# Kernel tuning notes

Hardware: AMD Instinct MI355X
Metric: run time of the kernel (lower is better)

Reference implementation:

```python
import jax, jax.numpy as jnp
import numpy as np

LN_EPS = 1e-5


def conv2d(x, w, b, stride, pad):
    # x: NCHW, w: OIHW
    y = jax.lax.conv_general_dilated(
        x, w, (stride, stride), [(pad, pad), (pad, pad)],
        dimension_numbers=("NCHW", "OIHW", "NCHW"))
    return y + b[None, :, None, None]


def gdn(x, gamma, beta):
    # y_c = x_c / sqrt(beta_c + sum_j gamma_cj * x_j^2)  (1x1 conv on x^2)
    norm = jnp.einsum("bchw,dc->bdhw", x * x, gamma) + beta[None, :, None, None]
    return x / jnp.sqrt(norm)


def layernorm(x, w, b):
    mu = jnp.mean(x, axis=-1, keepdims=True)
    var = jnp.var(x, axis=-1, keepdims=True)
    return (x - mu) / jnp.sqrt(var + LN_EPS) * w + b


def setup_inputs() -> dict:
    key = jax.random.key(0)
    ks = jax.random.split(key, 16)
    r = lambda i, shape: (jax.random.normal(ks[i], shape) * 0.02).astype(jnp.float32)
    N, M, K, D = 128, 192, 192, 128
    return {
        "x_p": jax.random.normal(ks[0], (4, 16, 3, 64, 64), jnp.float32),
        "y_g": jax.random.normal(ks[1], (64, K, 32), jnp.float32),
        "conv1_w": r(2, (N, 3, 5, 5)), "conv1_b": jnp.zeros((N,), jnp.float32),
        "gamma1": (0.1 * jnp.eye(N) + 1e-3).astype(jnp.float32), "beta1": jnp.ones((N,), jnp.float32),
        "conv2_w": r(3, (N, N, 5, 5)), "conv2_b": jnp.zeros((N,), jnp.float32),
        "gamma2": (0.1 * jnp.eye(N) + 1e-3).astype(jnp.float32), "beta2": jnp.ones((N,), jnp.float32),
        "conv3_w": r(4, (M, N, 3, 3)), "conv3_b": jnp.zeros((M,), jnp.float32),
        "ln_q_w": jnp.ones((M,), jnp.float32), "ln_q_b": jnp.zeros((M,), jnp.float32),
        "ln_kv_w": jnp.ones((K,), jnp.float32), "ln_kv_b": jnp.zeros((K,), jnp.float32),
        "ln_out_w": jnp.ones((M,), jnp.float32), "ln_out_b": jnp.zeros((M,), jnp.float32),
        "Wq": r(5, (D, M)), "Wk": r(6, (D, K)), "v_w": r(7, (1, D)),
        "Wv": r(8, (M, K)), "out_w": r(9, (M, M)), "out_b": jnp.zeros((M,), jnp.float32),
    }


def reference(x_p, y_g, conv1_w, conv1_b, gamma1, beta1, conv2_w, conv2_b,
              gamma2, beta2, conv3_w, conv3_b, ln_q_w, ln_q_b, ln_kv_w, ln_kv_b,
              ln_out_w, ln_out_b, Wq, Wk, v_w, Wv, out_w, out_b):
    B, P, C, Hp, Wp = x_p.shape
    x = x_p.reshape(B * P, C, Hp, Wp)
    # local encoder: conv s2 -> GDN -> conv s2 -> GDN -> conv s1 k3
    x = gdn(conv2d(x, conv1_w, conv1_b, 2, 2), gamma1, beta1)
    x = gdn(conv2d(x, conv2_w, conv2_b, 2, 2), gamma2, beta2)
    y_local = conv2d(x, conv3_w, conv3_b, 1, 1)          # (BP, M, h, w)
    BP, M, h, w = y_local.shape
    q = y_local.reshape(BP, M, h * w).transpose(0, 2, 1)  # (BP, Tq, M)
    kv = y_g.reshape(BP, y_g.shape[1], -1).transpose(0, 2, 1)  # (BP, Tk, K)
    q = layernorm(q, ln_q_w, ln_q_b)
    kv = layernorm(kv, ln_kv_w, ln_kv_b)
    # Bahdanau additive attention
    q_proj = jnp.einsum("bqm,dm->bqd", q, Wq)            # (BP, Tq, D)
    k_proj = jnp.einsum("bkc,dc->bkd", kv, Wk)           # (BP, Tk, D)
    energy = jnp.einsum("bqkd,d->bqk",
                        jnp.tanh(q_proj[:, :, None, :] + k_proj[:, None, :, :]),
                        v_w[0])                           # (BP, Tq, Tk)
    alpha = jax.nn.softmax(energy, axis=-1)
    v_proj = jnp.einsum("bkc,mc->bkm", kv, Wv)           # (BP, Tk, M)
    context = jnp.einsum("bqk,bkm->bqm", alpha, v_proj)
    context = jnp.einsum("bqm,nm->bqn", context, out_w) + out_b
    fused = layernorm(q + context, ln_out_w, ln_out_b)
    return fused.transpose(0, 2, 1).reshape(BP, M, h, w)
```

## Files before the change

kernel.cpp:

```cpp
#include <hip/hip_runtime.h>
#include <cstddef>
#include <cstdint>


typedef __bf16 bf16x8 __attribute__((ext_vector_type(8)));
typedef float floatx4 __attribute__((ext_vector_type(4)));
typedef unsigned short ushortT;
typedef unsigned short ushort8v __attribute__((ext_vector_type(8)));

#if __has_builtin(__builtin_amdgcn_exp2f)
#define EXP2F(x) __builtin_amdgcn_exp2f(x)
#else
#define EXP2F(x) exp2f(x)
#endif
#if __has_builtin(__builtin_amdgcn_rcpf)
#define RCPF(x) __builtin_amdgcn_rcpf(x)
#else
#define RCPF(x) (1.f / (x))
#endif

__device__ __forceinline__ ushortT f2bf(float f) {
  unsigned u = __builtin_bit_cast(unsigned, f);
  unsigned r = (u + 0x7FFFu + ((u >> 16) & 1u)) >> 16;
  return (ushortT)r;
}
__device__ __forceinline__ float bf2f(ushortT u) {
  return __builtin_bit_cast(float, ((unsigned)u) << 16);
}

static constexpr size_t OFF_T1BF = 0;
static constexpr size_t OFF_X2BF = 4194304;
static constexpr size_t OFF_T2BF = 8388608;
static constexpr size_t OFF_X3BF = 9437184;
static constexpr size_t OFF_QRAW = 10485760;
static constexpr size_t OFF_WBQ  = 21299200;
static constexpr size_t OFF_WBK  = 21311488;
static constexpr size_t OFF_WBV  = 21323776;
static constexpr size_t OFF_WBO  = 21342208;
static constexpr size_t OFF_WT2  = 26079232;
static constexpr size_t OFF_WT3  = 26284032;
static constexpr size_t OFF_WC1  = 26394624;
static constexpr size_t OFF_GB1  = 26406912;
static constexpr size_t OFF_GB2  = 26415104;
static constexpr size_t OFF_KP   = OFF_T1BF;
static constexpr size_t OFF_VT   = OFF_T1BF + 262144;

__device__ __constant__ int d_TWI2[4][9] = {{ 0, 2, 4,10,12,14,20,22,24},
                                            { 1, 3,11,13,21,23, 0, 0, 0},
                                            { 5, 7, 9,15,17,19, 0, 0, 0},
                                            { 6, 8,16,18, 0, 0, 0, 0, 0}};
__device__ __constant__ int d_NT2[4] = {9, 6, 6, 4};

__device__ void dev_convw3(const float* w, ushortT* wt, int mode, int total,
                           int idx) {
  if (idx >= total) return;
  int j    = idx & 7;
  int om   = (idx >> 3) & 63;
  int kg   = (idx >> 9) & 3;
  int slab = idx >> 11;
  int mt, s, tap, T;
  if (mode == 0) {
    int ph;
    if (slab < 72) ph = 0; else if (slab < 120) ph = 1;
    else if (slab < 168) ph = 2; else ph = 3;
    const int st[4] = {0, 72, 120, 168};
    const int ns[4] = {36, 24, 24, 16};
    int rel = slab - st[ph];
    mt = rel / ns[ph]; s = rel % ns[ph];
    tap = d_TWI2[ph][s >> 2]; T = 25;
  } else {
    mt = slab / 36; s = slab % 36; tap = s >> 2; T = 9;
  }
  int cc = s & 3;
  int c  = cc * 32 + kg * 8 + j;
  int oc = mt * 64 + om;
  wt[idx] = f2bf(w[(size_t)(oc * 128 + c) * T + tap]);
}

__device__ void dev_convw1(const float* w, ushortT* wt, int idx) {
  if (idx >= 20480) return;
  int k    = idx & 31;
  int oc   = (idx >> 5) & 127;
  int slab = idx >> 12;
  int ph, i;
  if (slab < 2) { ph = 0; i = slab; } else { ph = slab - 1; i = 0; }
  int kg = k >> 3, jj = k & 7;
  int tidx = i * 8 + jj;
  float val = 0.f;
  if (kg < 3 && tidx < d_NT2[ph]) {
    int tap = d_TWI2[ph][tidx];
    val = w[(size_t)(oc * 3 + kg) * 25 + tap];
  }
  wt[idx] = f2bf(val);
}

__device__ void dev_wcast(const float* w, ushortT* wb, int total, float scale,
                          int idx) {
  if (idx < total) wb[idx] = f2bf(w[idx] * scale);
}

__global__ __launch_bounds__(256) void prep_kernel(
    const float* __restrict__ conv2_w, ushortT* __restrict__ wt2,
    const float* __restrict__ conv3_w, ushortT* __restrict__ wt3,
    const float* __restrict__ conv1_w, ushortT* __restrict__ wc1,
    const float* __restrict__ Wq, ushortT* __restrict__ wbq,
    const float* __restrict__ Wk, ushortT* __restrict__ wbk,
    const float* __restrict__ Wv, ushortT* __restrict__ wbv,
    const float* __restrict__ out_w, ushortT* __restrict__ wbo,
    const float* __restrict__ gamma1, ushortT* __restrict__ gb1,
    const float* __restrict__ gamma2, ushortT* __restrict__ gb2) {
  constexpr float C2LE = 2.88539008177792681f;
  int blk = blockIdx.x, tid = threadIdx.x;
  if (blk < 1600)      dev_convw3(conv2_w, wt2, 0, 409600, blk * 256 + tid);
  else if (blk < 2464) dev_convw3(conv3_w, wt3, 1, 221184, (blk - 1600) * 256 + tid);
  else if (blk < 2544) dev_convw1(conv1_w, wc1, (blk - 2464) * 256 + tid);
  else if (blk < 2640) dev_wcast(Wq, wbq, 24576, C2LE, (blk - 2544) * 256 + tid);
  else if (blk < 2736) dev_wcast(Wk, wbk, 24576, C2LE, (blk - 2640) * 256 + tid);
  else if (blk < 2880) dev_wcast(Wv, wbv, 36864, 1.f, (blk - 2736) * 256 + tid);
  else if (blk < 3024) dev_wcast(out_w, wbo, 36864, 1.f, (blk - 2880) * 256 + tid);
  else if (blk < 3088) dev_wcast(gamma1, gb1, 16384, 1.f, (blk - 3024) * 256 + tid);
  else                 dev_wcast(gamma2, gb2, 16384, 1.f, (blk - 3088) * 256 + tid);
}

__global__ __launch_bounds__(256, 1) void conv1_mfma_kernel(
    const float* __restrict__ x, const ushortT* __restrict__ wc1,
    const float* __restrict__ bias, ushortT* __restrict__ outb) {
  int b  = blockIdx.x >> 2;
  int yg = blockIdx.x & 3;
  int y0 = yg * 8;

  int wave = threadIdx.x >> 6;
  int lane = threadIdx.x & 63;
  int ln15 = lane & 15;
  int kg   = lane >> 4;
  int tid  = threadIdx.x;

  __shared__ ushortT simg[4680];
  __shared__ ushortT sA[5 * 128 * 40];

  for (int j = tid; j < 2340; j += 256) ((unsigned*)simg)[j] = 0u;
  __syncthreads();

  int ihBase = 2 * y0 - 2;
  const float* xb = x + (size_t)b * 3 * 4096;
  for (int j = tid; j < 960; j += 256) {
    int q = j & 15;
    int rr = j >> 4;
    int c = rr / 20, ihl = rr % 20;
    int ih = ihBase + ihl;
    if (ih >= 0 && ih < 64) {
      float4 v = *(const float4*)&xb[c * 4096 + ih * 64 + q * 4];
      int pr = ih & 1, u = ih >> 1;
      int lr = u - y0 + 1;
      int base0 = ((pr * 2 + 0) * 3 + c) * 360 + lr * 36;
      int base1 = ((pr * 2 + 1) * 3 + c) * 360 + lr * 36;
      simg[base0 + 2 * q + 1] = f2bf(v.x);
      simg[base1 + 2 * q + 1] = f2bf(v.y);
      simg[base0 + 2 * q + 2] = f2bf(v.z);
      simg[base1 + 2 * q + 2] = f2bf(v.w);
    }
  }
  for (int j = tid; j < 2560; j += 256) {
    int chunk = j & 3, row = j >> 2;
    uint4 v = *(const uint4*)&wc1[row * 32 + chunk * 8];
    *(uint4*)&sA[row * 40 + chunk * 8] = v;
  }
  __syncthreads();

  constexpr int TDR[4][9] = {{-1,-1,-1, 0, 0, 0, 1, 1, 1},
                             {-1,-1, 0, 0, 1, 1, 0, 0, 0},
                             {-1,-1,-1, 0, 0, 0, 0, 0, 0},
                             {-1,-1, 0, 0, 0, 0, 0, 0, 0}};
  constexpr int TDC[4][9] = {{-1, 0, 1,-1, 0, 1,-1, 0, 1},
                             {-1, 0,-1, 0,-1, 0, 0, 0, 0},
                             {-1, 0, 1,-1, 0, 1, 0, 0, 0},
                             {-1, 0,-1, 0, 0, 0, 0, 0, 0}};
  constexpr int NT[4]  = {9, 6, 6, 4};
  constexpr int NM[4]  = {2, 1, 1, 1};
  constexpr int SB[4]  = {0, 2, 3, 4};

  ushort8v Bf[4][5];
  #pragma unroll
  for (int ntl = 0; ntl < 4; ++ntl) {
    int ntg = wave * 4 + ntl;
    int yloc = ntg >> 1;
    int xx = (ntg & 1) * 16 + ln15;
    int lbase = (yloc + 1) * 36 + xx + 1 + kg * 360;
    #pragma unroll
    for (int ph = 0; ph < 4; ++ph) {
      int pbase = ph * 1080 + lbase;
      #pragma unroll
      for (int i = 0; i < 2; ++i) {
        if (i < NM[ph]) {
          ushort8v bv;
          #pragma unroll
          for (int j = 0; j < 8; ++j) {
            int tidx = i * 8 + j;
            if (tidx >= NT[ph]) tidx = 0;
            int off = TDR[ph][tidx] * 36 + TDC[ph][tidx];
            bv[j] = simg[pbase + off];
          }
          Bf[ntl][SB[ph] + i] = bv;
        }
      }
    }
  }

  #pragma unroll
  for (int m = 0; m < 8; ++m) {
    bf16x8 Af[5];
    #pragma unroll
    for (int s = 0; s < 5; ++s)
      Af[s] = *(const bf16x8*)&sA[(s * 128 + m * 16 + ln15) * 40 + kg * 8];
    int oc0 = m * 16 + kg * 4;
    float4 bv = *(const float4*)&bias[oc0];
    #pragma unroll
    for (int ntl = 0; ntl < 4; ++ntl) {
      floatx4 acc = (floatx4)0.f;
      #pragma unroll
      for (int s = 0; s < 5; ++s)
        acc = __builtin_amdgcn_mfma_f32_16x16x32_bf16(
            Af[s], __builtin_bit_cast(bf16x8, Bf[ntl][s]), acc, 0, 0, 0);
      int ntg = wave * 4 + ntl;
      int y = y0 + (ntg >> 1);
      int xx = (ntg & 1) * 16 + ln15;
      int p = y * 32 + xx;
      ushort4 o4 = {f2bf(acc[0] + bv.x), f2bf(acc[1] + bv.y),
                    f2bf(acc[2] + bv.z), f2bf(acc[3] + bv.w)};
      *(ushort4*)&outb[((size_t)b * 1024 + p) * 128 + oc0] = o4;
    }
  }
}

__global__ __launch_bounds__(256) void gdn_mfma_kernel(
    const ushortT* __restrict__ xbf, const ushortT* __restrict__ gb,
    const float* __restrict__ beta, ushortT* __restrict__ ybf,
    int HW, int nPixTiles, int isSplit) {
  int pt = blockIdx.x % nPixTiles;
  int b  = blockIdx.x / nPixTiles;
  int px0 = pt * 64;
  int tid = threadIdx.x;
  int wave = tid >> 6, lane = tid & 63, ln15 = lane & 15, kg = lane >> 4;

  __shared__ ushortT sG[128 * 136];
  __shared__ ushortT sX[64 * 136];

  for (int j = tid; j < 2048; j += 256) {
    int row = j >> 4, ch = j & 15;
    *(uint4*)&sG[row * 136 + ch * 8] = *(const uint4*)&gb[row * 128 + ch * 8];
  }
  for (int j = tid; j < 1024; j += 256) {
    int row = j >> 4, ch = j & 15;
    ushort8v xv = *(const ushort8v*)&xbf[((size_t)(b * HW + px0 + row)) * 128 + ch * 8];
    ushort8v sq;
    #pragma unroll
    for (int r = 0; r < 8; ++r) {
      float f = bf2f(xv[r]);
      sq[r] = f2bf(f * f);
    }
    *(ushort8v*)&sX[row * 136 + ch * 8] = sq;
  }
  __syncthreads();

  floatx4 acc[2][4];
  #pragma unroll
  for (int mi = 0; mi < 2; ++mi)
    #pragma unroll
    for (int nt = 0; nt < 4; ++nt) acc[mi][nt] = (floatx4)0.f;

  #pragma unroll
  for (int k0 = 0; k0 < 128; k0 += 32) {
    bf16x8 a0 = *(const bf16x8*)&sG[(wave * 32 + ln15) * 136 + k0 + kg * 8];
    bf16x8 a1 = *(const bf16x8*)&sG[(wave * 32 + 16 + ln15) * 136 + k0 + kg * 8];
    #pragma unroll
    for (int nt = 0; nt < 4; ++nt) {
      bf16x8 bb = *(const bf16x8*)&sX[(nt * 16 + ln15) * 136 + k0 + kg * 8];
      acc[0][nt] = __builtin_amdgcn_mfma_f32_16x16x32_bf16(a0, bb, acc[0][nt], 0, 0, 0);
      acc[1][nt] = __builtin_amdgcn_mfma_f32_16x16x32_bf16(a1, bb, acc[1][nt], 0, 0, 0);
    }
  }

  #pragma unroll
  for (int mi = 0; mi < 2; ++mi) {
    int d0 = wave * 32 + mi * 16 + kg * 4;
    float4 bt = *(const float4*)&beta[d0];
    #pragma unroll
    for (int nt = 0; nt < 4; ++nt) {
      int p = px0 + nt * 16 + ln15;
      ushort4 x4 = *(const ushort4*)&xbf[((size_t)(b * HW + p)) * 128 + d0];
      ushort4 o4;
      o4.x = f2bf(bf2f(x4.x) * rsqrtf(acc[mi][nt][0] + bt.x));
      o4.y = f2bf(bf2f(x4.y) * rsqrtf(acc[mi][nt][1] + bt.y));
      o4.z = f2bf(bf2f(x4.z) * rsqrtf(acc[mi][nt][2] + bt.z));
      o4.w = f2bf(bf2f(x4.w) * rsqrtf(acc[mi][nt][3] + bt.w));
      size_t dst;
      if (isSplit) {
        int h = p >> 5, w5 = p & 31;
        int ph = ((h & 1) << 1) | (w5 & 1);
        dst = (((size_t)b * 4 + ph) * 256 + (h >> 1) * 16 + (w5 >> 1)) * 128 + d0;
      } else {
        dst = ((size_t)b * 256 + p) * 128 + d0;
      }
      *(ushort4*)&ybf[dst] = o4;
    }
  }
}

template<int MODE>
__global__ __launch_bounds__(256, 2) void conv_mfma_kernel(
    const ushortT* __restrict__ X,
    const ushortT* __restrict__ Wt,
    const float* __restrict__ bias,
    ushortT* __restrict__ outb) {
  constexpr int OC  = (MODE == 0) ? 128 : 192;
  constexpr int NMT = OC / 64;
  constexpr int NPH = (MODE == 0) ? 4 : 1;

  int b   = blockIdx.x / (NMT * 4);
  int rem = blockIdx.x % (NMT * 4);
  int mt  = rem >> 2;
  int rs  = rem & 3;
  int r0  = rs * 4;

  int wave = threadIdx.x >> 6;
  int lane = threadIdx.x & 63;
  int ln15 = lane & 15;
  int kg   = lane >> 4;

  __shared__ ushortT simg[6 * 18 * 136];

  floatx4 acc[4];
  #pragma unroll
  for (int m = 0; m < 4; ++m) acc[m] = (floatx4)0.f;

  constexpr int NS2[4]      = {36, 24, 24, 16};
  constexpr int PHSTART2[4] = {0, 72, 120, 168};
  constexpr int TDR_2[4][9] = {{-1,-1,-1, 0, 0, 0, 1, 1, 1},
                               {-1,-1, 0, 0, 1, 1, 0, 0, 0},
                               {-1,-1,-1, 0, 0, 0, 0, 0, 0},
                               {-1,-1, 0, 0, 0, 0, 0, 0, 0}};
  constexpr int TDC_2[4][9] = {{-1, 0, 1,-1, 0, 1,-1, 0, 1},
                               {-1, 0,-1, 0,-1, 0, 0, 0, 0},
                               {-1, 0, 1,-1, 0, 1, 0, 0, 0},
                               {-1, 0,-1, 0, 0, 0, 0, 0, 0}};
  constexpr int TDR_3[9] = {-1,-1,-1, 0, 0, 0, 1, 1, 1};
  constexpr int TDC_3[9] = {-1, 0, 1,-1, 0, 1,-1, 0, 1};

  const int aoff = kg * 512 + ln15 * 8;
  uint4 apf[8][4];

  #pragma unroll
  for (int ph = 0; ph < NPH; ++ph) {
    const int NS = (MODE == 0) ? NS2[ph] : 36;
    const int slabBase = (MODE == 0) ? (PHSTART2[ph] + mt * NS2[ph]) : (mt * 36);
    const ushortT* wp0 = Wt + (size_t)slabBase * 2048 + aoff;

    __syncthreads();
    const ushortT* Xb = X + (((size_t)b * NPH + ph) * 256) * 128;
    for (int idx = threadIdx.x; idx < 1728; idx += 256) {
      int chunk = idx & 15;
      int pix = idx >> 4;
      int row = pix / 18, colm = pix - row * 18;
      int i = r0 - 1 + row, j = colm - 1;
      uint4 v = {0u, 0u, 0u, 0u};
      if (i >= 0 && i < 16 && j >= 0 && j < 16)
        v = *(const uint4*)(Xb + ((size_t)(i * 16 + j)) * 128 + chunk * 8);
      *(uint4*)&simg[(row * 18 + colm) * 136 + chunk * 8] = v;
    }
    #pragma unroll
    for (int jj = 0; jj < 8; ++jj)
      if (jj < NS) {
        #pragma unroll
        for (int m = 0; m < 4; ++m)
          apf[jj][m] = *(const uint4*)(wp0 + (size_t)jj * 2048 + m * 128);
      }
    __syncthreads();

    #pragma unroll
    for (int s0 = 0; s0 < NS; s0 += 8) {
      #pragma unroll
      for (int jj = 0; jj < 8; ++jj) {
        int s = s0 + jj;
        if (s < NS) {
          bf16x8 acur[4];
          #pragma unroll
          for (int m = 0; m < 4; ++m) acur[m] = __builtin_bit_cast(bf16x8, apf[jj][m]);
          int sp = s + 8;
          if (sp < NS) {
            #pragma unroll
            for (int m = 0; m < 4; ++m)
              apf[jj][m] = *(const uint4*)(wp0 + (size_t)sp * 2048 + m * 128);
          }
          int t  = s >> 2;
          int c0 = (s & 3) * 32;
          int dr = (MODE == 0) ? TDR_2[ph][t] : TDR_3[t];
          int dc = (MODE == 0) ? TDC_2[ph][t] : TDC_3[t];
          int lrow = wave + dr + 1;
          int lcol = ln15 + dc + 1;
          bf16x8 bfr = *(const bf16x8*)&simg[(lrow * 18 + lcol) * 136 + c0 + kg * 8];
          #pragma unroll
          for (int m = 0; m < 4; ++m)
            acc[m] = __builtin_amdgcn_mfma_f32_16x16x32_bf16(acur[m], bfr, acc[m], 0, 0, 0);
        }
      }
    }
  }

  #pragma unroll
  for (int m = 0; m < 4; ++m) {
    int mg = mt * 64 + m * 16 + kg * 4;
    float4 bv = *(const float4*)&bias[mg];
    int r = r0 + wave;
    int p = r * 16 + ln15;
    ushort4 o4 = {f2bf(acc[m][0] + bv.x), f2bf(acc[m][1] + bv.y),
                  f2bf(acc[m][2] + bv.z), f2bf(acc[m][3] + bv.w)};
    *(ushort4*)&outb[((size_t)b * 256 + p) * OC + mg] = o4;
  }
}

__global__ __launch_bounds__(256) void kv_prep_kernel(
    const float* __restrict__ yg, const float* __restrict__ ln_kv_w,
    const float* __restrict__ ln_kv_b, const ushortT* __restrict__ wbk,
    const ushortT* __restrict__ wbv, float* __restrict__ kp,
    ushortT* __restrict__ vT) {
  __shared__ float skvRaw[32 * 194];
  __shared__ ushortT skv[32 * 200];
  int b = blockIdx.x;
  int tid = threadIdx.x;
  int wave = tid >> 6, lane = tid & 63, ln15 = lane & 15, kg = lane >> 4;

  const float4* yg4 = (const float4*)(yg + (size_t)b * 6144);
  for (int j = tid; j < 1536; j += 256) {
    float4 v = yg4[j];
    int c = j >> 3;
    int t4 = (j & 7) * 4;
    skvRaw[(t4 + 0) * 194 + c] = v.x;
    skvRaw[(t4 + 1) * 194 + c] = v.y;
    skvRaw[(t4 + 2) * 194 + c] = v.z;
    skvRaw[(t4 + 3) * 194 + c] = v.w;
  }
  __syncthreads();
  for (int r = wave; r < 32; r += 4) {
    const float* src = skvRaw + r * 194;
    float v0 = src[lane], v1 = src[lane + 64], v2 = src[lane + 128];
    float s = v0 + v1 + v2;
    float s2 = v0 * v0 + v1 * v1 + v2 * v2;
    #pragma unroll
    for (int off = 32; off; off >>= 1) { s += __shfl_xor(s, off); s2 += __shfl_xor(s2, off); }
    float mean = s * (1.f / 192.f);
    float var = s2 * (1.f / 192.f) - mean * mean;
    float inv = rsqrtf(var + 1e-5f);
    skv[r * 200 + lane]       = f2bf((v0 - mean) * inv * ln_kv_w[lane]       + ln_kv_b[lane]);
    skv[r * 200 + lane + 64]  = f2bf((v1 - mean) * inv * ln_kv_w[lane + 64]  + ln_kv_b[lane + 64]);
    skv[r * 200 + lane + 128] = f2bf((v2 - mean) * inv * ln_kv_w[lane + 128] + ln_kv_b[lane + 128]);
  }
  __syncthreads();
  for (int ti = wave; ti < 40; ti += 4) {
    floatx4 acc = (floatx4)0.f;
    if (ti < 16) {
      int rt = ti >> 3, ct = ti & 7;
      #pragma unroll
      for (int k0 = 0; k0 < 192; k0 += 32) {
        bf16x8 afr = *(const bf16x8*)&skv[(rt * 16 + ln15) * 200 + k0 + kg * 8];
        bf16x8 bfr = *(const bf16x8*)&wbk[((size_t)(ct * 16 + ln15)) * 192 + k0 + kg * 8];
        acc = __builtin_amdgcn_mfma_f32_16x16x32_bf16(afr, bfr, acc, 0, 0, 0);
      }
      #pragma unroll
      for (int r = 0; r < 4; ++r)
        kp[((size_t)b * 32 + rt * 16 + kg * 4 + r) * 128 + ct * 16 + ln15] = acc[r];
    } else {
      int t2 = ti - 16;
      int rt = t2 / 12, ct = t2 % 12;
      #pragma unroll
      for (int k0 = 0; k0 < 192; k0 += 32) {
        bf16x8 afr = *(const bf16x8*)&skv[(rt * 16 + ln15) * 200 + k0 + kg * 8];
        bf16x8 bfr = *(const bf16x8*)&wbv[((size_t)(ct * 16 + ln15)) * 192 + k0 + kg * 8];
        acc = __builtin_amdgcn_mfma_f32_16x16x32_bf16(afr, bfr, acc, 0, 0, 0);
      }
      #pragma unroll
      for (int r = 0; r < 4; ++r)
        vT[((size_t)b * 192 + ct * 16 + ln15) * 32 + rt * 16 + kg * 4 + r] = f2bf(acc[r]);
    }
  }
}

__global__ __launch_bounds__(256) void attn_kernel(
    const ushortT* __restrict__ qrawb, const float* __restrict__ ln_q_w,
    const float* __restrict__ ln_q_b, const float* __restrict__ kp,
    const ushortT* __restrict__ vT, const ushortT* __restrict__ wbq,
    const ushortT* __restrict__ wbo, const float* __restrict__ vw,
    const float* __restrict__ out_b, const float* __restrict__ ln_out_w,
    const float* __restrict__ ln_out_b, float* __restrict__ out) {
  __shared__ ushortT smem[17284];
  ushortT* sqln = smem;
  float*   skp  = (float*)(smem + 3200);
  float*   sqpF = (float*)(smem + 11648);
  float*   se   = (float*)(smem + 15872);
  float*   swm  = (float*)(smem + 17024);
  float*   sS0  = (float*)(smem + 17280);
  ushortT* sctx = smem;
  float*   sf   = (float*)(smem + 3200);

  int b  = blockIdx.x >> 4;
  int t0 = (blockIdx.x & 15) * 16;
  int tid  = threadIdx.x;
  int wave = tid >> 6;
  int lane = tid & 63;
  int ln15 = lane & 15;
  int kg   = lane >> 4;

  {
    const float4* kp4 = (const float4*)(kp + (size_t)b * 4096);
    for (int j = tid; j < 1024; j += 256) {
      int row = j >> 5, c4 = j & 31;
      *(float4*)&skp[row * 132 + c4 * 4] = kp4[j];
    }
  }
  for (int r = wave; r < 16; r += 4) {
    const ushortT* xr = qrawb + ((size_t)(b * 256 + t0 + r)) * 192;
    float v0 = bf2f(xr[lane]), v1 = bf2f(xr[lane + 64]), v2 = bf2f(xr[lane + 128]);
    float s = v0 + v1 + v2;
    float s2 = v0 * v0 + v1 * v1 + v2 * v2;
    #pragma unroll
    for (int off = 32; off; off >>= 1) { s += __shfl_xor(s, off); s2 += __shfl_xor(s2, off); }
    float mean = s * (1.f / 192.f);
    float var = s2 * (1.f / 192.f) - mean * mean;
    float inv = rsqrtf(var + 1e-5f);
    sqln[r * 200 + lane]       = f2bf((v0 - mean) * inv * ln_q_w[lane]       + ln_q_b[lane]);
    sqln[r * 200 + lane + 64]  = f2bf((v1 - mean) * inv * ln_q_w[lane + 64]  + ln_q_b[lane + 64]);
    sqln[r * 200 + lane + 128] = f2bf((v2 - mean) * inv * ln_q_w[lane + 128] + ln_q_b[lane + 128]);
  }
  if (tid < 128) swm[tid] = -2.f * vw[tid];
  if (tid >= 128 && tid < 192) {
    int l = tid - 128;
    float s = vw[l] + vw[l + 64];
    #pragma unroll
    for (int off = 32; off; off >>= 1) s += __shfl_xor(s, off);
    if (l == 0) *sS0 = s;
  }
  __syncthreads();

  for (int ti = wave; ti < 8; ti += 4) {
    floatx4 acc = (floatx4)0.f;
    #pragma unroll
    for (int k0 = 0; k0 < 192; k0 += 32) {
      bf16x8 afr = *(const bf16x8*)&sqln[ln15 * 200 + k0 + kg * 8];
      bf16x8 bfr = *(const bf16x8*)&wbq[((size_t)(ti * 16 + ln15)) * 192 + k0 + kg * 8];
      acc = __builtin_amdgcn_mfma_f32_16x16x32_bf16(afr, bfr, acc, 0, 0, 0);
    }
    #pragma unroll
    for (int r = 0; r < 4; ++r)
      sqpF[(kg * 4 + r) * 132 + ti * 16 + ln15] = acc[r];
  }
  __syncthreads();

  {
    float S0v = *sS0;
    int qq = tid >> 4, kc = tid & 15;
    const float4* w4 = (const float4*)swm;
    const float4* q4 = (const float4*)&sqpF[qq * 132];
    const float4* ka = (const float4*)&skp[kc * 132];
    const float4* kb = (const float4*)&skp[(kc + 16) * 132];
    float acc0 = S0v, acc1 = S0v;
    #pragma unroll 8
    for (int d4 = 0; d4 < 32; ++d4) {
      float4 qv = q4[d4], k0v = ka[d4], k1v = kb[d4], wv = w4[d4];
      acc0 += wv.x * RCPF(EXP2F(qv.x + k0v.x) + 1.f);
      acc0 += wv.y * RCPF(EXP2F(qv.y + k0v.y) + 1.f);
      acc0 += wv.z * RCPF(EXP2F(qv.z + k0v.z) + 1.f);
      acc0 += wv.w * RCPF(EXP2F(qv.w + k0v.w) + 1.f);
      acc1 += wv.x * RCPF(EXP2F(qv.x + k1v.x) + 1.f);
      acc1 += wv.y * RCPF(EXP2F(qv.y + k1v.y) + 1.f);
      acc1 += wv.z * RCPF(EXP2F(qv.z + k1v.z) + 1.f);
      acc1 += wv.w * RCPF(EXP2F(qv.w + k1v.w) + 1.f);
    }
    float mx = fmaxf(acc0, acc1);
    #pragma unroll
    for (int off = 8; off; off >>= 1) mx = fmaxf(mx, __shfl_xor(mx, off));
    float e0 = __expf(acc0 - mx), e1 = __expf(acc1 - mx);
    float s = e0 + e1;
    #pragma unroll
    for (int off = 8; off; off >>= 1) s += __shfl_xor(s, off);
    float inv = 1.f / s;
    se[qq * 36 + kc]      = e0 * inv;
    se[qq * 36 + kc + 16] = e1 * inv;
  }
  __syncthreads();

  {
    float4 a0 = *(const float4*)&se[ln15 * 36 + kg * 8];
    float4 a1 = *(const float4*)&se[ln15 * 36 + kg * 8 + 4];
    ushort8v au;
    au[0] = f2bf(a0.x); au[1] = f2bf(a0.y); au[2] = f2bf(a0.z); au[3] = f2bf(a0.w);
    au[4] = f2bf(a1.x); au[5] = f2bf(a1.y); au[6] = f2bf(a1.z); au[7] = f2bf(a1.w);
    for (int ti = wave; ti < 12; ti += 4) {
      bf16x8 bfr = *(const bf16x8*)&vT[((size_t)(b * 192 + ti * 16 + ln15)) * 32 + kg * 8];
      floatx4 acc = __builtin_amdgcn_mfma_f32_16x16x32_bf16(
          __builtin_bit_cast(bf16x8, au), bfr, (floatx4)0.f, 0, 0, 0);
      #pragma unroll
      for (int r = 0; r < 4; ++r)
        sctx[(kg * 4 + r) * 200 + ti * 16 + ln15] = f2bf(acc[r]);
    }
  }
  __syncthreads();

  for (int ti = wave; ti < 12; ti += 4) {
    floatx4 acc = (floatx4)0.f;
    #pragma unroll
    for (int k0 = 0; k0 < 192; k0 += 32) {
      bf16x8 afr = *(const bf16x8*)&sctx[ln15 * 200 + k0 + kg * 8];
      bf16x8 bfr = *(const bf16x8*)&wbo[((size_t)(ti * 16 + ln15)) * 192 + k0 + kg * 8];
      acc = __builtin_amdgcn_mfma_f32_16x16x32_bf16(afr, bfr, acc, 0, 0, 0);
    }
    float bv = out_b[ti * 16 + ln15];
    #pragma unroll
    for (int r = 0; r < 4; ++r)
      sf[(kg * 4 + r) * 193 + ti * 16 + ln15] = acc[r] + bv;
  }
  __syncthreads();

  for (int rr = wave; rr < 16; rr += 4) {
    int t = t0 + rr;
    const ushortT* xr = qrawb + ((size_t)(b * 256 + t)) * 192;
    float r0_ = bf2f(xr[lane]), r1_ = bf2f(xr[lane + 64]), r2_ = bf2f(xr[lane + 128]);
    float s = r0_ + r1_ + r2_;
    float s2 = r0_ * r0_ + r1_ * r1_ + r2_ * r2_;
    #pragma unroll
    for (int off = 32; off; off >>= 1) { s += __shfl_xor(s, off); s2 += __shfl_xor(s2, off); }
    float mean = s * (1.f / 192.f);
    float var = s2 * (1.f / 192.f) - mean * mean;
    float inv = rsqrtf(var + 1e-5f);
    float q0 = (r0_ - mean) * inv * ln_q_w[lane]       + ln_q_b[lane];
    float q1 = (r1_ - mean) * inv * ln_q_w[lane + 64]  + ln_q_b[lane + 64];
    float q2 = (r2_ - mean) * inv * ln_q_w[lane + 128] + ln_q_b[lane + 128];
    float v0 = sf[rr * 193 + lane]       + q0;
    float v1 = sf[rr * 193 + lane + 64]  + q1;
    float v2 = sf[rr * 193 + lane + 128] + q2;
    float t_s = v0 + v1 + v2;
    float t_s2 = v0 * v0 + v1 * v1 + v2 * v2;
    #pragma unroll
    for (int off = 32; off; off >>= 1) { t_s += __shfl_xor(t_s, off); t_s2 += __shfl_xor(t_s2, off); }
    float m2 = t_s * (1.f / 192.f);
    float var2 = t_s2 * (1.f / 192.f) - m2 * m2;
    float inv2 = rsqrtf(var2 + 1e-5f);
    sf[rr * 193 + lane]       = (v0 - m2) * inv2 * ln_out_w[lane]       + ln_out_b[lane];
    sf[rr * 193 + lane + 64]  = (v1 - m2) * inv2 * ln_out_w[lane + 64]  + ln_out_b[lane + 64];
    sf[rr * 193 + lane + 128] = (v2 - m2) * inv2 * ln_out_w[lane + 128] + ln_out_b[lane + 128];
  }
  __syncthreads();

  for (int j = tid; j < 768; j += 256) {
    int m = j >> 2, t4 = j & 3;
    float4 o4;
    o4.x = sf[(t4 * 4 + 0) * 193 + m];
    o4.y = sf[(t4 * 4 + 1) * 193 + m];
    o4.z = sf[(t4 * 4 + 2) * 193 + m];
    o4.w = sf[(t4 * 4 + 3) * 193 + m];
    *(float4*)&out[((size_t)(b * 192 + m)) * 256 + t0 + t4 * 4] = o4;
  }
}

extern "C" void kernel_launch(void* const* d_in, const int* in_sizes, int n_in,
                              void* d_out, int out_size, void* d_ws, size_t ws_size,
                              hipStream_t stream) {
  (void)in_sizes; (void)n_in; (void)out_size; (void)ws_size;
  const float* x_p     = (const float*)d_in[0];
  const float* y_g     = (const float*)d_in[1];
  const float* conv1_w = (const float*)d_in[2];
  const float* conv1_b = (const float*)d_in[3];
  const float* gamma1  = (const float*)d_in[4];
  const float* beta1   = (const float*)d_in[5];
  const float* conv2_w = (const float*)d_in[6];
  const float* conv2_b = (const float*)d_in[7];
  const float* gamma2  = (const float*)d_in[8];
  const float* beta2   = (const float*)d_in[9];
  const float* conv3_w = (const float*)d_in[10];
  const float* conv3_b = (const float*)d_in[11];
  const float* ln_q_w  = (const float*)d_in[12];
  const float* ln_q_b  = (const float*)d_in[13];
  const float* ln_kv_w = (const float*)d_in[14];
  const float* ln_kv_b = (const float*)d_in[15];
  const float* ln_out_w= (const float*)d_in[16];
  const float* ln_out_b= (const float*)d_in[17];
  const float* Wq      = (const float*)d_in[18];
  const float* Wk      = (const float*)d_in[19];
  const float* v_w     = (const float*)d_in[20];
  const float* Wv      = (const float*)d_in[21];
  const float* out_w   = (const float*)d_in[22];
  const float* out_b   = (const float*)d_in[23];
  float* out = (float*)d_out;
  float* ws  = (float*)d_ws;

  ushortT* t1bf  = (ushortT*)(ws + OFF_T1BF);
  ushortT* x2bf  = (ushortT*)(ws + OFF_X2BF);
  ushortT* t2bf  = (ushortT*)(ws + OFF_T2BF);
  ushortT* x3bf  = (ushortT*)(ws + OFF_X3BF);
  ushortT* qrawb = (ushortT*)(ws + OFF_QRAW);
  ushortT* wbq   = (ushortT*)(ws + OFF_WBQ);
  ushortT* wbk   = (ushortT*)(ws + OFF_WBK);
  ushortT* wbv   = (ushortT*)(ws + OFF_WBV);
  ushortT* wbo   = (ushortT*)(ws + OFF_WBO);
  ushortT* wt2   = (ushortT*)(ws + OFF_WT2);
  ushortT* wt3   = (ushortT*)(ws + OFF_WT3);
  ushortT* wc1   = (ushortT*)(ws + OFF_WC1);
  ushortT* gb1   = (ushortT*)(ws + OFF_GB1);
  ushortT* gb2   = (ushortT*)(ws + OFF_GB2);
  float*   kp    = (float*)(ws + OFF_KP);
  ushortT* vTb   = (ushortT*)(ws + OFF_VT);

  prep_kernel<<<3152, 256, 0, stream>>>(conv2_w, wt2, conv3_w, wt3, conv1_w, wc1,
                                        Wq, wbq, Wk, wbk, Wv, wbv, out_w, wbo,
                                        gamma1, gb1, gamma2, gb2);
  conv1_mfma_kernel<<<256, 256, 0, stream>>>(x_p, wc1, conv1_b, t1bf);
  gdn_mfma_kernel<<<1024, 256, 0, stream>>>(t1bf, gb1, beta1, x2bf, 1024, 16, 1);
  conv_mfma_kernel<0><<<512, 256, 0, stream>>>(x2bf, wt2, conv2_b, t2bf);
  gdn_mfma_kernel<<<256, 256, 0, stream>>>(t2bf, gb2, beta2, x3bf, 256, 4, 0);
  conv_mfma_kernel<1><<<768, 256, 0, stream>>>(x3bf, wt3, conv3_b, qrawb);
  kv_prep_kernel<<<64, 256, 0, stream>>>(y_g, ln_kv_w, ln_kv_b, wbk, wbv,
                                         kp, vTb);
  attn_kernel<<<1024, 256, 0, stream>>>(qrawb, ln_q_w, ln_q_b, kp, vTb,
                                        wbq, wbo, v_w, out_b, ln_out_w,
                                        ln_out_b, out);
}
```

Measured before the change: 241.0 us.

## Fuse GDN normalization into conv1 and conv2 epilogues

Measured after the change: 227.1 us. 1.06x faster.

```diff
diff --git a/kernel.cpp b/kernel.cpp
--- a/kernel.cpp
+++ b/kernel.cpp
@@ -28,9 +28,7 @@
   return __builtin_bit_cast(float, ((unsigned)u) << 16);
 }
 
-static constexpr size_t OFF_T1BF = 0;
 static constexpr size_t OFF_X2BF = 4194304;
-static constexpr size_t OFF_T2BF = 8388608;
 static constexpr size_t OFF_X3BF = 9437184;
 static constexpr size_t OFF_QRAW = 10485760;
 static constexpr size_t OFF_WBQ  = 21299200;
@@ -42,8 +40,8 @@
 static constexpr size_t OFF_WC1  = 26394624;
 static constexpr size_t OFF_GB1  = 26406912;
 static constexpr size_t OFF_GB2  = 26415104;
-static constexpr size_t OFF_KP   = OFF_T1BF;
-static constexpr size_t OFF_VT   = OFF_T1BF + 262144;
+static constexpr size_t OFF_KP   = 0;
+static constexpr size_t OFF_VT   = 262144;
 
 __device__ __constant__ int d_TWI2[4][9] = {{ 0, 2, 4,10,12,14,20,22,24},
                                             { 1, 3,11,13,21,23, 0, 0, 0},
@@ -122,9 +120,10 @@
   else                 dev_wcast(gamma2, gb2, 16384, 1.f, (blk - 3088) * 256 + tid);
 }
 
-__global__ __launch_bounds__(256, 1) void conv1_mfma_kernel(
+__global__ __launch_bounds__(256, 1) void conv1_gdn_kernel(
     const float* __restrict__ x, const ushortT* __restrict__ wc1,
-    const float* __restrict__ bias, ushortT* __restrict__ outb) {
+    const float* __restrict__ bias, const ushortT* __restrict__ gb1,
+    const float* __restrict__ beta1, ushortT* __restrict__ outb) {
   int b  = blockIdx.x >> 2;
   int yg = blockIdx.x & 3;
   int y0 = yg * 8;
@@ -135,8 +134,9 @@
   int kg   = lane >> 4;
   int tid  = threadIdx.x;
 
-  __shared__ ushortT simg[4680];
-  __shared__ ushortT sA[5 * 128 * 40];
+  __shared__ ushortT smem[30280];
+  ushortT* simg = smem;
+  ushortT* sA   = smem + 4680;
 
   for (int j = tid; j < 2340; j += 256) ((unsigned*)simg)[j] = 0u;
   __syncthreads();
@@ -206,6 +206,7 @@
     }
   }
 
+  ushort4 xq[8][4];
   #pragma unroll
   for (int m = 0; m < 8; ++m) {
     bf16x8 Af[5];
@@ -221,113 +222,82 @@
       for (int s = 0; s < 5; ++s)
         acc = __builtin_amdgcn_mfma_f32_16x16x32_bf16(
             Af[s], __builtin_bit_cast(bf16x8, Bf[ntl][s]), acc, 0, 0, 0);
-      int ntg = wave * 4 + ntl;
-      int y = y0 + (ntg >> 1);
-      int xx = (ntg & 1) * 16 + ln15;
-      int p = y * 32 + xx;
       ushort4 o4 = {f2bf(acc[0] + bv.x), f2bf(acc[1] + bv.y),
                     f2bf(acc[2] + bv.z), f2bf(acc[3] + bv.w)};
-      *(ushort4*)&outb[((size_t)b * 1024 + p) * 128 + oc0] = o4;
-    }
-  }
-}
-
-__global__ __launch_bounds__(256) void gdn_mfma_kernel(
-    const ushortT* __restrict__ xbf, const ushortT* __restrict__ gb,
-    const float* __restrict__ beta, ushortT* __restrict__ ybf,
-    int HW, int nPixTiles, int isSplit) {
-  int pt = blockIdx.x % nPixTiles;
-  int b  = blockIdx.x / nPixTiles;
-  int px0 = pt * 64;
-  int tid = threadIdx.x;
-  int wave = tid >> 6, lane = tid & 63, ln15 = lane & 15, kg = lane >> 4;
-
-  __shared__ ushortT sG[128 * 136];
-  __shared__ ushortT sX[64 * 136];
+      xq[m][ntl] = o4;
+    }
+  }
+  __syncthreads();
 
   for (int j = tid; j < 2048; j += 256) {
     int row = j >> 4, ch = j & 15;
-    *(uint4*)&sG[row * 136 + ch * 8] = *(const uint4*)&gb[row * 128 + ch * 8];
-  }
-  for (int j = tid; j < 1024; j += 256) {
-    int row = j >> 4, ch = j & 15;
-    ushort8v xv = *(const ushort8v*)&xbf[((size_t)(b * HW + px0 + row)) * 128 + ch * 8];
-    ushort8v sq;
-    #pragma unroll
-    for (int r = 0; r < 8; ++r) {
-      float f = bf2f(xv[r]);
-      sq[r] = f2bf(f * f);
-    }
-    *(ushort8v*)&sX[row * 136 + ch * 8] = sq;
-  }
-  __syncthreads();
-
-  floatx4 acc[2][4];
+    *(uint4*)&smem[row * 136 + ch * 8] = *(const uint4*)&gb1[row * 128 + ch * 8];
+  }
+  __syncthreads();
+
+  const int sxbase = 17408 + wave * 2176;
   #pragma unroll
-  for (int mi = 0; mi < 2; ++mi)
-    #pragma unroll
-    for (int nt = 0; nt < 4; ++nt) acc[mi][nt] = (floatx4)0.f;
-
-  #pragma unroll
-  for (int k0 = 0; k0 < 128; k0 += 32) {
-    bf16x8 a0 = *(const bf16x8*)&sG[(wave * 32 + ln15) * 136 + k0 + kg * 8];
-    bf16x8 a1 = *(const bf16x8*)&sG[(wave * 32 + 16 + ln15) * 136 + k0 + kg * 8];
-    #pragma unroll
-    for (int nt = 0; nt < 4; ++nt) {
-      bf16x8 bb = *(const bf16x8*)&sX[(nt * 16 + ln15) * 136 + k0 + kg * 8];
-      acc[0][nt] = __builtin_amdgcn_mfma_f32_16x16x32_bf16(a0, bb, acc[0][nt], 0, 0, 0);
-      acc[1][nt] = __builtin_amdgcn_mfma_f32_16x16x32_bf16(a1, bb, acc[1][nt], 0, 0, 0);
-    }
-  }
-
-  #pragma unroll
-  for (int mi = 0; mi < 2; ++mi) {
-    int d0 = wave * 32 + mi * 16 + kg * 4;
-    float4 bt = *(const float4*)&beta[d0];
-    #pragma unroll
-    for (int nt = 0; nt < 4; ++nt) {
-      int p = px0 + nt * 16 + ln15;
-      ushort4 x4 = *(const ushort4*)&xbf[((size_t)(b * HW + p)) * 128 + d0];
+  for (int q = 0; q < 4; ++q) {
+    #pragma unroll
+    for (int m = 0; m < 8; ++m) {
+      ushort4 xv = xq[m][q];
+      float f0 = bf2f(xv.x), f1 = bf2f(xv.y), f2 = bf2f(xv.z), f3 = bf2f(xv.w);
+      ushort4 s4 = {f2bf(f0 * f0), f2bf(f1 * f1), f2bf(f2 * f2), f2bf(f3 * f3)};
+      *(ushort4*)&smem[sxbase + ln15 * 136 + m * 16 + kg * 4] = s4;
+    }
+    __syncthreads();
+    int ntg = wave * 4 + q;
+    int y = y0 + (ntg >> 1);
+    int xx = (ntg & 1) * 16 + ln15;
+    int ph = ((y & 1) << 1) | (xx & 1);
+    size_t dstbase = (((size_t)b * 4 + ph) * 256 + (y >> 1) * 16 + (xx >> 1)) * 128;
+    #pragma unroll
+    for (int dt = 0; dt < 8; ++dt) {
+      floatx4 acc = (floatx4)0.f;
+      #pragma unroll
+      for (int k0 = 0; k0 < 4; ++k0) {
+        bf16x8 ga = *(const bf16x8*)&smem[(dt * 16 + ln15) * 136 + k0 * 32 + kg * 8];
+        bf16x8 xbv = *(const bf16x8*)&smem[sxbase + ln15 * 136 + k0 * 32 + kg * 8];
+        acc = __builtin_amdgcn_mfma_f32_16x16x32_bf16(ga, xbv, acc, 0, 0, 0);
+      }
+      int d0 = dt * 16 + kg * 4;
+      float4 bt = *(const float4*)&beta1[d0];
+      ushort4 xv = xq[dt][q];
       ushort4 o4;
-      o4.x = f2bf(bf2f(x4.x) * rsqrtf(acc[mi][nt][0] + bt.x));
-      o4.y = f2bf(bf2f(x4.y) * rsqrtf(acc[mi][nt][1] + bt.y));
-      o4.z = f2bf(bf2f(x4.z) * rsqrtf(acc[mi][nt][2] + bt.z));
-      o4.w = f2bf(bf2f(x4.w) * rsqrtf(acc[mi][nt][3] + bt.w));
-      size_t dst;
-      if (isSplit) {
-        int h = p >> 5, w5 = p & 31;
-        int ph = ((h & 1) << 1) | (w5 & 1);
-        dst = (((size_t)b * 4 + ph) * 256 + (h >> 1) * 16 + (w5 >> 1)) * 128 + d0;
-      } else {
-        dst = ((size_t)b * 256 + p) * 128 + d0;
-      }
-      *(ushort4*)&ybf[dst] = o4;
-    }
-  }
-}
-
-template<int MODE>
-__global__ __launch_bounds__(256, 2) void conv_mfma_kernel(
-    const ushortT* __restrict__ X,
-    const ushortT* __restrict__ Wt,
-    const float* __restrict__ bias,
-    ushortT* __restrict__ outb) {
-  constexpr int OC  = (MODE == 0) ? 128 : 192;
-  constexpr int NMT = OC / 64;
-  constexpr int NPH = (MODE == 0) ? 4 : 1;
-
-  int b   = blockIdx.x / (NMT * 4);
-  int rem = blockIdx.x % (NMT * 4);
-  int mt  = rem >> 2;
-  int rs  = rem & 3;
-  int r0  = rs * 4;
+      o4.x = f2bf(bf2f(xv.x) * rsqrtf(acc[0] + bt.x));
+      o4.y = f2bf(bf2f(xv.y) * rsqrtf(acc[1] + bt.y));
+      o4.z = f2bf(bf2f(xv.z) * rsqrtf(acc[2] + bt.z));
+      o4.w = f2bf(bf2f(xv.w) * rsqrtf(acc[3] + bt.w));
+      *(ushort4*)&outb[dstbase + d0] = o4;
+    }
+    __syncthreads();
+  }
+}
+
+__global__ __launch_bounds__(256, 2) void conv2_gdn_kernel(
+    const ushortT* __restrict__ X, const ushortT* __restrict__ Wt,
+    const float* __restrict__ bias, const ushortT* __restrict__ gb2,
+    const float* __restrict__ beta2, ushortT* __restrict__ outb) {
+  int b  = blockIdx.x >> 3;
+  int rs = blockIdx.x & 7;
+  int r0 = rs * 2;
 
   int wave = threadIdx.x >> 6;
   int lane = threadIdx.x & 63;
   int ln15 = lane & 15;
   int kg   = lane >> 4;
-
-  __shared__ ushortT simg[6 * 18 * 136];
+  int wrow  = wave & 1;
+  int whalf = wave >> 1;
+
+  __shared__ ushortT smem[31552];
+  ushortT* simg = smem;
+  ushortT* sGam = smem + 9792;
+  ushortT* sX2  = smem + 27200;
+
+  for (int j = threadIdx.x; j < 2048; j += 256) {
+    int row = j >> 4, ch = j & 15;
+    *(uint4*)&sGam[row * 136 + ch * 8] = *(const uint4*)&gb2[row * 128 + ch * 8];
+  }
 
   floatx4 acc[4];
   #pragma unroll
@@ -343,21 +313,18 @@
                                {-1, 0,-1, 0,-1, 0, 0, 0, 0},
                                {-1, 0, 1,-1, 0, 1, 0, 0, 0},
                                {-1, 0,-1, 0, 0, 0, 0, 0, 0}};
-  constexpr int TDR_3[9] = {-1,-1,-1, 0, 0, 0, 1, 1, 1};
-  constexpr int TDC_3[9] = {-1, 0, 1,-1, 0, 1,-1, 0, 1};
 
   const int aoff = kg * 512 + ln15 * 8;
   uint4 apf[8][4];
 
   #pragma unroll
-  for (int ph = 0; ph < NPH; ++ph) {
-    const int NS = (MODE == 0) ? NS2[ph] : 36;
-    const int slabBase = (MODE == 0) ? (PHSTART2[ph] + mt * NS2[ph]) : (mt * 36);
-    const ushortT* wp0 = Wt + (size_t)slabBase * 2048 + aoff;
+  for (int ph = 0; ph < 4; ++ph) {
+    const int NS = NS2[ph];
+    const ushortT* wp0 = Wt + (size_t)(PHSTART2[ph] + whalf * NS) * 2048 + aoff;
 
     __syncthreads();
-    const ushortT* Xb = X + (((size_t)b * NPH + ph) * 256) * 128;
-    for (int idx = threadIdx.x; idx < 1728; idx += 256) {
+    const ushortT* Xb = X + (((size_t)b * 4 + ph) * 256) * 128;
+    for (int idx = threadIdx.x; idx < 1152; idx += 256) {
       int chunk = idx & 15;
       int pix = idx >> 4;
       int row = pix / 18, colm = pix - row * 18;
@@ -368,12 +335,11 @@
       *(uint4*)&simg[(row * 18 + colm) * 136 + chunk * 8] = v;
     }
     #pragma unroll
-    for (int jj = 0; jj < 8; ++jj)
-      if (jj < NS) {
-        #pragma unroll
-        for (int m = 0; m < 4; ++m)
-          apf[jj][m] = *(const uint4*)(wp0 + (size_t)jj * 2048 + m * 128);
-      }
+    for (int jj = 0; jj < 8; ++jj) {
+      #pragma unroll
+      for (int m = 0; m < 4; ++m)
+        apf[jj][m] = *(const uint4*)(wp0 + (size_t)jj * 2048 + m * 128);
+    }
     __syncthreads();
 
     #pragma unroll
@@ -393,10 +359,130 @@
           }
           int t  = s >> 2;
           int c0 = (s & 3) * 32;
-          int dr = (MODE == 0) ? TDR_2[ph][t] : TDR_3[t];
-          int dc = (MODE == 0) ? TDC_2[ph][t] : TDC_3[t];
-          int lrow = wave + dr + 1;
+          int dr = TDR_2[ph][t];
+          int dc = TDC_2[ph][t];
+          int lrow = wrow + dr + 1;
           int lcol = ln15 + dc + 1;
+          bf16x8 bfr = *(const bf16x8*)&simg[(lrow * 18 + lcol) * 136 + c0 + kg * 8];
+          #pragma unroll
+          for (int m = 0; m < 4; ++m)
+            acc[m] = __builtin_amdgcn_mfma_f32_16x16x32_bf16(acur[m], bfr, acc[m], 0, 0, 0);
+        }
+      }
+    }
+  }
+
+  ushort4 xq2[4];
+  #pragma unroll
+  for (int m = 0; m < 4; ++m) {
+    int mg = whalf * 64 + m * 16 + kg * 4;
+    float4 bv = *(const float4*)&bias[mg];
+    ushort4 o4 = {f2bf(acc[m][0] + bv.x), f2bf(acc[m][1] + bv.y),
+                  f2bf(acc[m][2] + bv.z), f2bf(acc[m][3] + bv.w)};
+    xq2[m] = o4;
+    float f0 = bf2f(o4.x), f1 = bf2f(o4.y), f2 = bf2f(o4.z), f3 = bf2f(o4.w);
+    ushort4 s4 = {f2bf(f0 * f0), f2bf(f1 * f1), f2bf(f2 * f2), f2bf(f3 * f3)};
+    *(ushort4*)&sX2[(wrow * 16 + ln15) * 136 + mg] = s4;
+  }
+  __syncthreads();
+
+  int p = (r0 + wrow) * 16 + ln15;
+  size_t obase = ((size_t)b * 256 + p) * 128;
+  #pragma unroll
+  for (int dti = 0; dti < 4; ++dti) {
+    int dt = whalf * 4 + dti;
+    floatx4 nacc = (floatx4)0.f;
+    #pragma unroll
+    for (int k0 = 0; k0 < 4; ++k0) {
+      bf16x8 ga = *(const bf16x8*)&sGam[(dt * 16 + ln15) * 136 + k0 * 32 + kg * 8];
+      bf16x8 xbv = *(const bf16x8*)&sX2[(wrow * 16 + ln15) * 136 + k0 * 32 + kg * 8];
+      nacc = __builtin_amdgcn_mfma_f32_16x16x32_bf16(ga, xbv, nacc, 0, 0, 0);
+    }
+    int d0 = dt * 16 + kg * 4;
+    float4 bt = *(const float4*)&beta2[d0];
+    ushort4 xv = xq2[dti];
+    ushort4 o4;
+    o4.x = f2bf(bf2f(xv.x) * rsqrtf(nacc[0] + bt.x));
+    o4.y = f2bf(bf2f(xv.y) * rsqrtf(nacc[1] + bt.y));
+    o4.z = f2bf(bf2f(xv.z) * rsqrtf(nacc[2] + bt.z));
+    o4.w = f2bf(bf2f(xv.w) * rsqrtf(nacc[3] + bt.w));
+    *(ushort4*)&outb[obase + d0] = o4;
+  }
+}
+
+__global__ __launch_bounds__(256, 2) void conv3_mfma_kernel(
+    const ushortT* __restrict__ X,
+    const ushortT* __restrict__ Wt,
+    const float* __restrict__ bias,
+    ushortT* __restrict__ outb) {
+  constexpr int OC  = 192;
+  constexpr int NMT = 3;
+
+  int b   = blockIdx.x / (NMT * 4);
+  int rem = blockIdx.x % (NMT * 4);
+  int mt  = rem >> 2;
+  int rs  = rem & 3;
+  int r0  = rs * 4;
+
+  int wave = threadIdx.x >> 6;
+  int lane = threadIdx.x & 63;
+  int ln15 = lane & 15;
+  int kg   = lane >> 4;
+
+  __shared__ ushortT simg[6 * 18 * 136];
+
+  floatx4 acc[4];
+  #pragma unroll
+  for (int m = 0; m < 4; ++m) acc[m] = (floatx4)0.f;
+
+  constexpr int TDR_3[9] = {-1,-1,-1, 0, 0, 0, 1, 1, 1};
+  constexpr int TDC_3[9] = {-1, 0, 1,-1, 0, 1,-1, 0, 1};
+
+  const int aoff = kg * 512 + ln15 * 8;
+  uint4 apf[8][4];
+
+  {
+    const int NS = 36;
+    const ushortT* wp0 = Wt + (size_t)(mt * 36) * 2048 + aoff;
+
+    const ushortT* Xb = X + ((size_t)b * 256) * 128;
+    for (int idx = threadIdx.x; idx < 1728; idx += 256) {
+      int chunk = idx & 15;
+      int pix = idx >> 4;
+      int row = pix / 18, colm = pix - row * 18;
+      int i = r0 - 1 + row, j = colm - 1;
+      uint4 v = {0u, 0u, 0u, 0u};
+      if (i >= 0 && i < 16 && j >= 0 && j < 16)
+        v = *(const uint4*)(Xb + ((size_t)(i * 16 + j)) * 128 + chunk * 8);
+      *(uint4*)&simg[(row * 18 + colm) * 136 + chunk * 8] = v;
+    }
+    #pragma unroll
+    for (int jj = 0; jj < 8; ++jj) {
+      #pragma unroll
+      for (int m = 0; m < 4; ++m)
+        apf[jj][m] = *(const uint4*)(wp0 + (size_t)jj * 2048 + m * 128);
+    }
+    __syncthreads();
+
+    #pragma unroll
+    for (int s0 = 0; s0 < NS; s0 += 8) {
+      #pragma unroll
+      for (int jj = 0; jj < 8; ++jj) {
+        int s = s0 + jj;
+        if (s < NS) {
+          bf16x8 acur[4];
+          #pragma unroll
+          for (int m = 0; m < 4; ++m) acur[m] = __builtin_bit_cast(bf16x8, apf[jj][m]);
+          int sp = s + 8;
+          if (sp < NS) {
+            #pragma unroll
+            for (int m = 0; m < 4; ++m)
+              apf[jj][m] = *(const uint4*)(wp0 + (size_t)sp * 2048 + m * 128);
+          }
+          int t  = s >> 2;
+          int c0 = (s & 3) * 32;
+          int lrow = wave + TDR_3[t] + 1;
+          int lcol = ln15 + TDC_3[t] + 1;
           bf16x8 bfr = *(const bf16x8*)&simg[(lrow * 18 + lcol) * 136 + c0 + kg * 8];
           #pragma unroll
           for (int m = 0; m < 4; ++m)
@@ -691,9 +777,7 @@
   float* out = (float*)d_out;
   float* ws  = (float*)d_ws;
 
-  ushortT* t1bf  = (ushortT*)(ws + OFF_T1BF);
   ushortT* x2bf  = (ushortT*)(ws + OFF_X2BF);
-  ushortT* t2bf  = (ushortT*)(ws + OFF_T2BF);
   ushortT* x3bf  = (ushortT*)(ws + OFF_X3BF);
   ushortT* qrawb = (ushortT*)(ws + OFF_QRAW);
   ushortT* wbq   = (ushortT*)(ws + OFF_WBQ);
@@ -711,13 +795,11 @@
   prep_kernel<<<3152, 256, 0, stream>>>(conv2_w, wt2, conv3_w, wt3, conv1_w, wc1,
                                         Wq, wbq, Wk, wbk, Wv, wbv, out_w, wbo,
                                         gamma1, gb1, gamma2, gb2);
-  conv1_mfma_kernel<<<256, 256, 0, stream>>>(x_p, wc1, conv1_b, t1bf);
-  gdn_mfma_kernel<<<1024, 256, 0, stream>>>(t1bf, gb1, beta1, x2bf, 1024, 16, 1);
-  conv_mfma_kernel<0><<<512, 256, 0, stream>>>(x2bf, wt2, conv2_b, t2bf);
-  gdn_mfma_kernel<<<256, 256, 0, stream>>>(t2bf, gb2, beta2, x3bf, 256, 4, 0);
-  conv_mfma_kernel<1><<<768, 256, 0, stream>>>(x3bf, wt3, conv3_b, qrawb);
   kv_prep_kernel<<<64, 256, 0, stream>>>(y_g, ln_kv_w, ln_kv_b, wbk, wbv,
                                          kp, vTb);
+  conv1_gdn_kernel<<<256, 256, 0, stream>>>(x_p, wc1, conv1_b, gb1, beta1, x2bf);
+  conv2_gdn_kernel<<<512, 256, 0, stream>>>(x2bf, wt2, conv2_b, gb2, beta2, x3bf);
+  conv3_mfma_kernel<<<768, 256, 0, stream>>>(x3bf, wt3, conv3_b, qrawb);
   attn_kernel<<<1024, 256, 0, stream>>>(qrawb, ln_q_w, ln_q_b, kp, vTb,
                                         wbq, wbo, v_w, out_b, ln_out_w,
                                         ln_out_b, out);
```
